# Optimization experiments

Measured on AMD Instinct MI355X. Metric: run time of the kernel, lower is better.

Reference implementation:

```python
import jax, jax.numpy as jnp
import numpy as np
import math

B, TQ, TK = 64, 1024, 512
CONV_CH, EMBED_DIM, ATT_HID = 512, 512, 512
KEY_POS_RATE = 1.385
QUERY_POS_RATE = 1.0
POSITION_WEIGHT = 1.0


def sin_pos_enc(positions, w, d):
    # positions: [B, T] int, padding_idx=0 maps to zero vector.
    # pe[..., 2i]   = sin(w*pos / 10000^(2i/d))
    # pe[..., 2i+1] = cos(w*pos / 10000^(2i/d))
    i = jnp.arange(d)
    inv_freq = jnp.power(jnp.float32(10000.0), -(2.0 * (i // 2).astype(jnp.float32)) / d)  # [d]
    ang = (positions.astype(jnp.float32) * w)[..., None] * inv_freq  # [B, T, d]
    pe = jnp.where(i % 2 == 0, jnp.sin(ang), jnp.cos(ang))
    return jnp.where((positions == 0)[..., None], jnp.float32(0.0), pe)


def setup_inputs() -> dict:
    key = jax.random.key(0)
    ks = jax.random.split(key, 12)
    s = 0.02
    inp = {
        "query": jax.random.normal(ks[0], (B, TQ, CONV_CH), jnp.float32),
        "keys": jax.random.normal(ks[1], (B, TK, EMBED_DIM), jnp.float32),
        "values": jax.random.normal(ks[2], (B, TK, EMBED_DIM), jnp.float32),
        # 1-based positions (0 is the padding index of SinusoidalEncoding)
        "text_positions": jnp.broadcast_to(jnp.arange(1, TK + 1, dtype=jnp.int64), (B, TK)),
        "frame_positions": jnp.broadcast_to(jnp.arange(1, TQ + 1, dtype=jnp.int64), (B, TQ)),
        # pad mask over keys: last 64 text positions are padding
        "mask": jnp.broadcast_to(jnp.arange(TK) >= (TK - 64), (B, TK)),
        "Wq": jax.random.normal(ks[3], (CONV_CH, ATT_HID), jnp.float32) * s,
        "bq": jnp.zeros((ATT_HID,), jnp.float32),
        "Wk": jax.random.normal(ks[4], (EMBED_DIM, ATT_HID), jnp.float32) * s,
        "bk": jnp.zeros((ATT_HID,), jnp.float32),
        "Wv": jax.random.normal(ks[5], (EMBED_DIM, ATT_HID), jnp.float32) * s,
        "bv": jnp.zeros((ATT_HID,), jnp.float32),
        "Wo": jax.random.normal(ks[6], (ATT_HID, CONV_CH), jnp.float32) * s,
        "bo": jnp.zeros((CONV_CH,), jnp.float32),
    }
    return inp


def reference(query, keys, values, text_positions, frame_positions, mask,
              Wq, bq, Wk, bk, Wv, bv, Wo, bo):
    # positional-bias injection (position_weight = 1.0)
    keys = keys + POSITION_WEIGHT * sin_pos_enc(text_positions, KEY_POS_RATE, EMBED_DIM)[:, :keys.shape[1], :]
    query = query + POSITION_WEIGHT * sin_pos_enc(frame_positions, QUERY_POS_RATE, CONV_CH)[:, :frame_positions.shape[-1], :]

    v = values @ Wv + bv            # [B, TK, H]
    k = keys @ Wk + bk              # [B, TK, H]
    q = query @ Wq + bq             # [B, TQ, H]

    scores = jnp.einsum('bqh,bkh->bqk', q, k)               # [B, TQ, TK]
    scores = jnp.where(mask[:, None, :], -jnp.inf, scores)
    attn = jax.nn.softmax(scores, axis=2)
    # dropout is a no-op in eval mode
    x = jnp.einsum('bqk,bkh->bqh', attn, v)
    x = x * jnp.float32(math.sqrt(1.0 / v.shape[1]))
    out = x @ Wo + bo               # [B, TQ, conv_channels]
    return out, attn
```

## Files before the change

### kernel.cpp

```cpp
#include <hip/hip_runtime.h>
#include <stdint.h>

#define DEVI __device__ __forceinline__

typedef __attribute__((ext_vector_type(4))) float     f4v;
typedef __attribute__((ext_vector_type(8))) _Float16  h8;
typedef __attribute__((ext_vector_type(4))) _Float16  h4;
typedef unsigned int  u32;

static constexpr int   TQ = 1024, TKN = 512;
static constexpr float KEY_RATE = 1.385f;
static constexpr float QRY_RATE = 1.0f;
static constexpr float SCALE    = 0.04419417382415922f;
static constexpr float INVC     = 0.05190512648261504f;

static constexpr size_t OFF_MM   = 0;
static constexpr size_t OFF_NT   = OFF_MM  + (size_t)512*512*2;
static constexpr size_t OFF_WOT  = OFF_NT  + (size_t)512*512*2;
static constexpr size_t OFF_PEQ  = OFF_WOT + (size_t)512*512*4;
static constexpr size_t OFF_W    = OFF_PEQ + (size_t)1024*512*4;
static constexpr size_t OFF_C    = OFF_W   + 512*4;
static constexpr size_t OFF_BQBK = OFF_C   + 512*4;
static constexpr size_t OFF_T    = OFF_BQBK + 256;
static constexpr size_t OFF_KP   = OFF_T   + (size_t)64*512*4;
static constexpr size_t OFF_MKT  = OFF_KP  + (size_t)64*512*512*2;
static constexpr size_t OFF_PT   = OFF_MKT + (size_t)64*512*512*2;
static constexpr size_t WS_NEED  = OFF_PT  + (size_t)64*512*512*2;
static constexpr size_t OFF_A16  = WS_NEED;
static constexpr size_t WS_BIG   = OFF_A16 + (size_t)64*1024*512*2;

#define WAITV(N) asm volatile("s_waitcnt vmcnt(" #N ")" ::: "memory")
#define WAITL()  asm volatile("s_waitcnt lgkmcnt(0)" ::: "memory")
#define SCHEDB() __builtin_amdgcn_sched_barrier(0)
#define BARRAW() __builtin_amdgcn_s_barrier()

DEVI f4v mfma16(h8 a, h8 b, f4v c) {
  return __builtin_amdgcn_mfma_f32_16x16x32_f16(a, b, c, 0, 0, 0);
}

DEVI void gld16(void* lds, const void* g) {
  __builtin_amdgcn_global_load_lds(
      (const __attribute__((address_space(1))) unsigned int*)g,
      (__attribute__((address_space(3))) unsigned int*)lds, 16, 0, 0);
}

DEVI void stage_B(char* Bbuf, const _Float16* B, int k0, int tid) {
#pragma unroll
  for (int it = 0; it < 4; ++it) {
    const int c = (it << 9) + tid;
    const int r = c >> 2, s = c & 3;
    const int sg = s ^ ((r >> 1) & 3);
    gld16(Bbuf + ((size_t)c << 4), B + (size_t)r * 512 + k0 + (sg << 3));
  }
}

DEVI void stage_A16(char* Abuf, const _Float16* A, int k0, int tid) {
  const int r = tid >> 2, s = tid & 3;
  const int sg = s ^ ((r >> 1) & 3);
  gld16(Abuf + ((size_t)tid << 4), A + (size_t)r * 512 + k0 + (sg << 3));
}

DEVI void loads_A32(f4v& x0, f4v& x1, const float* A, const float* add, int k0, int tid) {
  const int r = tid >> 2, c8 = (tid & 3) << 3;
  const float* p = A + (size_t)r * 512 + k0 + c8;
  x0 = *(const f4v*)p; x1 = *(const f4v*)(p + 4);
  if (add) {
    const float* q = add + (size_t)r * 512 + k0 + c8;
    x0 += *(const f4v*)q; x1 += *(const f4v*)(q + 4);
  }
}
DEVI void write_A32(char* Abuf, f4v x0, f4v x1, int tid) {
  const int r = tid >> 2;
  const int slot = (tid & 3) ^ ((r >> 1) & 3);
  h8 o;
#pragma unroll
  for (int i = 0; i < 4; ++i) { o[i] = (_Float16)x0[i]; o[4 + i] = (_Float16)x1[i]; }
  *(h8*)(Abuf + (r << 6) + (slot << 4)) = o;
}

DEVI void read_fragsA(const char* Ab, int wr, int lane, h8 (&a)[4]) {
  const int l15 = lane & 15, hi = lane >> 4;
#pragma unroll
  for (int mi = 0; mi < 4; ++mi) {
    const int r = wr * 64 + mi * 16 + l15;
    a[mi] = *(const h8*)(Ab + (r << 6) + ((hi ^ ((r >> 1) & 3)) << 4));
  }
}
DEVI void read_fragsB(const char* Bb, int wc, int lane, h8 (&b)[8]) {
  const int l15 = lane & 15, hi = lane >> 4;
#pragma unroll
  for (int nj = 0; nj < 8; ++nj) {
    const int g = wc * 128 + nj * 16 + l15;
    b[nj] = *(const h8*)(Bb + (g << 6) + ((hi ^ ((g >> 1) & 3)) << 4));
  }
}

#define MFMA_ALL(a, bf, acc)                                   \
  _Pragma("unroll") for (int mi = 0; mi < 4; ++mi)             \
  _Pragma("unroll") for (int nj = 0; nj < 8; ++nj)             \
      acc[mi][nj] = mfma16(a[mi], bf[nj], acc[mi][nj]);

#define REG_PIPELINE(As, Ad, Bs, acc)                                              \
  {                                                                                \
    char* const Abf[2] = {lds, lds + 8192};                                        \
    char* const Bbf[3] = {lds + 16384, lds + 49152, lds + 81920};                  \
    f4v xa0, xa1, xb0, xb1;                                                        \
    loads_A32(xa0, xa1, As, Ad, 0, tid);                                           \
    loads_A32(xb0, xb1, As, Ad, 32, tid);                                          \
    SCHEDB();                                                                      \
    stage_B(Bbf[0], Bs, 0, tid);                                                   \
    stage_B(Bbf[1], Bs, 32, tid);                                                  \
    WAITV(4);                                                                      \
    write_A32(Abf[0], xa0, xa1, tid);                                              \
    WAITL(); SCHEDB(); BARRAW(); SCHEDB();                                         \
    _Pragma("unroll")                                                              \
    for (int k = 0; k < 16; ++k) {                                                 \
      if (k < 14) {                                                                \
        if ((k & 1) == 0) { loads_A32(xa0, xa1, As, Ad, (k + 2) * 32, tid); }      \
        else              { loads_A32(xb0, xb1, As, Ad, (k + 2) * 32, tid); }      \
        SCHEDB();                                                                  \
        stage_B(Bbf[(k + 2) % 3], Bs, (k + 2) * 32, tid);                          \
      }                                                                            \
      h8 a[4], bf[8];                                                              \
      read_fragsA(Abf[k & 1], wr, lane, a);                                        \
      read_fragsB(Bbf[k % 3], wc, lane, bf);                                       \
      MFMA_ALL(a, bf, acc);                                                        \
      if (k < 15) {                                                                \
        if (k < 14) { WAITV(6); } else { WAITV(0); }                               \
        if ((k & 1) == 0) write_A32(Abf[1], xb0, xb1, tid);                        \
        else              write_A32(Abf[0], xa0, xa1, tid);                        \
        WAITL(); SCHEDB(); BARRAW(); SCHEDB();                                     \
      }                                                                            \
    }                                                                              \
  }

#define GLD_PIPELINE(As, Bs, acc)                                                  \
  {                                                                                \
    char* const Abf[3] = {lds, lds + 8192, lds + 16384};                           \
    char* const Bbf[3] = {lds + 24576, lds + 57344, lds + 90112};                  \
    stage_A16(Abf[0], As, 0, tid);  stage_B(Bbf[0], Bs, 0, tid);                   \
    stage_A16(Abf[1], As, 32, tid); stage_B(Bbf[1], Bs, 32, tid);                  \
    WAITV(5); SCHEDB(); BARRAW(); SCHEDB();                                        \
    _Pragma("unroll")                                                              \
    for (int k = 0; k < 16; ++k) {                                                 \
      if (k < 14) {                                                                \
        stage_A16(Abf[(k + 2) % 3], As, (k + 2) * 32, tid);                        \
        stage_B(Bbf[(k + 2) % 3], Bs, (k + 2) * 32, tid);                          \
      }                                                                            \
      h8 a[4], bf[8];                                                              \
      read_fragsA(Abf[k % 3], wr, lane, a);                                        \
      read_fragsB(Bbf[k % 3], wc, lane, bf);                                       \
      MFMA_ALL(a, bf, acc);                                                        \
      if (k < 14) { WAITV(5); } else if (k == 14) { WAITV(0); }                    \
      if (k < 15) { WAITL(); SCHEDB(); BARRAW(); SCHEDB(); }                       \
    }                                                                              \
  }

DEVI void stage_f32_A(char* Abuf, const float* A, int k0, int tid) {
#pragma unroll
  for (int it = 0; it < 2; ++it) {
    const int idx = (it << 9) + tid;
    const int r = idx >> 3, c4 = idx & 7;
    f4v x = *(const f4v*)(A + (size_t)r * 512 + k0 + (c4 << 2));
    h4 o;
#pragma unroll
    for (int i = 0; i < 4; ++i) o[i] = (_Float16)x[i];
    const int slot = (c4 >> 1) ^ ((r >> 1) & 3);
    *(h4*)(Abuf + (r << 6) + (slot << 4) + ((c4 & 1) << 3)) = o;
  }
}
DEVI void stage_f32_B(char* Bbuf, const float* B, int k0, int tid) {
#pragma unroll
  for (int it = 0; it < 8; ++it) {
    const int idx = (it << 9) + tid;
    const int r = idx >> 3, c4 = idx & 7;
    f4v x = *(const f4v*)(B + (size_t)r * 512 + k0 + (c4 << 2));
    h4 o;
#pragma unroll
    for (int i = 0; i < 4; ++i) o[i] = (_Float16)x[i];
    const int slot = (c4 >> 1) ^ ((r >> 1) & 3);
    *(h4*)(Bbuf + (r << 6) + (slot << 4) + ((c4 & 1) << 3)) = o;
  }
}

__global__ __launch_bounds__(256) void k_prepA(
    const float* __restrict__ Wk, const float* __restrict__ bq,
    const float* __restrict__ bk,
    const float* __restrict__ Wo,
    const void* __restrict__ fpos_raw,
    float* __restrict__ wvec, float* __restrict__ bqbk,
    float* __restrict__ PEQ, float* __restrict__ WoT) {
  const int bid = blockIdx.x, tid = threadIdx.x;
  if (bid < 128) {
    const int wid = tid >> 6, lane = tid & 63;
    const int row = bid * 4 + wid;
    const float* p = Wk + (size_t)row * 512 + lane * 8;
    const f4v a = *(const f4v*)p, c = *(const f4v*)(p + 4);
    const f4v b0 = *(const f4v*)(bq + lane * 8), b1 = *(const f4v*)(bq + lane * 8 + 4);
    float d = a[0]*b0[0]+a[1]*b0[1]+a[2]*b0[2]+a[3]*b0[3]
            + c[0]*b1[0]+c[1]*b1[1]+c[2]*b1[2]+c[3]*b1[3];
#pragma unroll
    for (int off = 32; off; off >>= 1) d += __shfl_xor(d, off);
    if (lane == 0) wvec[row] = d;
  } else if (bid == 128) {
    __shared__ float red[256];
    red[tid] = bq[tid] * bk[tid] + bq[tid + 256] * bk[tid + 256];
    __syncthreads();
    if (tid == 0) { float s = 0.f; for (int h = 0; h < 256; ++h) s += red[h]; bqbk[0] = s; }
  } else if (bid < 129 + 2048) {
    const u32* fp = (const u32*)fpos_raw;
    const bool is64 = (fp[1] == 0);
    const int t = (bid - 129) * 256 + tid;
    const int tq = t >> 9, d = t & 511;
    const int pos = (int)(is64 ? fp[2 * tq] : fp[tq]);
    float pe = 0.f;
    if (pos != 0) {
      const float invf = exp2f(-(float)(d >> 1) * INVC);
      const float ang  = ((float)pos * QRY_RATE) * invf;
      pe = (d & 1) ? cosf(ang) : sinf(ang);
    }
    PEQ[t] = pe;
  } else {
    __shared__ float t[32][33];
    const int local = bid - 2177;
    const int bx = local & 15, by = local >> 4;
    const int tx = tid & 31, ty = tid >> 5;
    const int x = bx * 32 + tx;
#pragma unroll
    for (int j = 0; j < 4; ++j)
      t[ty + 8 * j][tx] = Wo[(size_t)(by * 32 + ty + 8 * j) * 512 + x];
    __syncthreads();
    const int x2 = by * 32 + tx;
#pragma unroll
    for (int j = 0; j < 4; ++j)
      WoT[(size_t)(bx * 32 + ty + 8 * j) * 512 + x2] = t[tx][ty + 8 * j];
  }
}

__global__ __launch_bounds__(512) void k_prepB(
    const float* __restrict__ Wq, const float* __restrict__ Wk,
    const float* __restrict__ WoT, const float* __restrict__ Wv,
    const float* __restrict__ keys, const void* __restrict__ tpos_raw,
    const void* __restrict__ mask_raw,
    const float* __restrict__ wvec, const float* __restrict__ bqbk,
    const float* __restrict__ bv, const float* __restrict__ bo,
    _Float16* __restrict__ Mm, _Float16* __restrict__ Nt,
    _Float16* __restrict__ kp, float* __restrict__ tvec,
    float* __restrict__ cvec) {
  __shared__ char lds[40960];
  const int bid = blockIdx.x, tid = threadIdx.x;
  const int lane = tid & 63, wid = tid >> 6;
  if (bid < 8) {
    char *Ab = lds, *Bb = lds + 8192;
    const int wr = wid >> 2, wc = wid & 3;
    const int x = bid & 3, y = bid >> 2;
    const float* A = (y == 0 ? Wq : WoT) + (size_t)x * 128 * 512;
    const float* B = (y == 0 ? Wk : Wv);
    _Float16* out = (y == 0 ? Mm : Nt) + (size_t)x * 128 * 512;
    f4v acc[4][8] = {};
    for (int ks = 0; ks < 16; ++ks) {
      stage_f32_A(Ab, A, ks * 32, tid);
      stage_f32_B(Bb, B, ks * 32, tid);
      __syncthreads();
      h8 a[4], bf[8];
      read_fragsA(Ab, wr, lane, a);
      read_fragsB(Bb, wc, lane, bf);
      MFMA_ALL(a, bf, acc);
      __syncthreads();
    }
    const int l15 = lane & 15, hi = lane >> 4;
#pragma unroll
    for (int mi = 0; mi < 4; ++mi)
#pragma unroll
      for (int nj = 0; nj < 8; ++nj) {
        const int col = wc * 128 + nj * 16 + l15;
#pragma unroll
        for (int j = 0; j < 4; ++j) {
          const int row = wr * 64 + mi * 16 + hi * 4 + j;
          out[(size_t)row * 512 + col] = (_Float16)acc[mi][nj][j];
        }
      }
  } else if (bid < 4104) {
    const u32* tp = (const u32*)tpos_raw;
    const bool is64 = (tp[1] == 0);
    const int row = (bid - 8) * 8 + wid;
    const int pos = (int)(is64 ? tp[2 * row] : tp[row]);
    const int d0  = lane * 8;
    const float* src = keys + (size_t)row * 512 + d0;
    const f4v a = *(const f4v*)src, b = *(const f4v*)(src + 4);
    float x[8] = {a[0], a[1], a[2], a[3], b[0], b[1], b[2], b[3]};
    if (pos != 0) {
      const float pw = (float)pos * KEY_RATE;
#pragma unroll
      for (int u = 0; u < 4; ++u) {
        const float invf = exp2f(-(float)(lane * 4 + u) * INVC);
        const float ang  = pw * invf;
        x[2*u]   += sinf(ang);
        x[2*u+1] += cosf(ang);
      }
    }
    const f4v w0 = *(const f4v*)(wvec + d0), w1 = *(const f4v*)(wvec + d0 + 4);
    float dot = 0.f;
#pragma unroll
    for (int i = 0; i < 4; ++i) dot += x[i] * w0[i] + x[4+i] * w1[i];
#pragma unroll
    for (int off = 32; off; off >>= 1) dot += __shfl_xor(dot, off);
    if (lane == 0) {
      const u32* m32 = (const u32*)mask_raw;
      const bool is32 = (m32[448] != 0);
      const bool mk = is32 ? (m32[row] != 0)
                           : (((const unsigned char*)mask_raw)[row] != 0);
      tvec[row] = mk ? -1e30f : (dot + bqbk[0]);
    }
    h8 o;
#pragma unroll
    for (int i = 0; i < 8; ++i) o[i] = (_Float16)x[i];
    *(h8*)(kp + (size_t)row * 512 + d0) = o;
  } else {
    const int row = (bid - 4104) * 8 + wid;
    const float* p = WoT + (size_t)row * 512 + lane * 8;
    const f4v a = *(const f4v*)p, c = *(const f4v*)(p + 4);
    const f4v b0 = *(const f4v*)(bv + lane * 8), b1 = *(const f4v*)(bv + lane * 8 + 4);
    float d = a[0]*b0[0]+a[1]*b0[1]+a[2]*b0[2]+a[3]*b0[3]
            + c[0]*b1[0]+c[1]*b1[1]+c[2]*b1[2]+c[3]*b1[3];
#pragma unroll
    for (int off = 32; off; off >>= 1) d += __shfl_xor(d, off);
    if (lane == 0) cvec[row] = SCALE * d + bo[row];
  }
}

__global__ __launch_bounds__(512, 1) void k_mkpv(
    const _Float16* __restrict__ kp, const _Float16* __restrict__ Mm,
    const float* __restrict__ values, const _Float16* __restrict__ Nt,
    _Float16* __restrict__ MKt, _Float16* __restrict__ Pt) {
  __shared__ char lds[122880];
  const int bid = blockIdx.x, tid = threadIdx.x;
  const int lane = tid & 63, wid = tid >> 6;
  const int wr = wid >> 2, wc = wid & 3;
  const int l15 = lane & 15, hi = lane >> 4;
  f4v acc[4][8] = {};
  if (bid < 256) {
    const int tt = bid & 3, b = bid >> 2;
    const _Float16* As = kp + ((size_t)b * TKN + tt * 128) * 512;
    GLD_PIPELINE(As, Mm, acc);
    _Float16* Ob = MKt + (size_t)b * TKN * 512 + (size_t)tt * 128 * 512;
#pragma unroll
    for (int mi = 0; mi < 4; ++mi)
#pragma unroll
      for (int nj = 0; nj < 8; ++nj) {
        const int col = wc * 128 + nj * 16 + l15;
#pragma unroll
        for (int j = 0; j < 4; ++j) {
          const int row = wr * 64 + mi * 16 + hi * 4 + j;
          Ob[(size_t)row * 512 + col] = (_Float16)acc[mi][nj][j];
        }
      }
  } else {
    const int rt = (bid - 256) & 3, b = (bid - 256) >> 2;
    const float* As = values + ((size_t)b * TKN + rt * 128) * 512;
    const float* Ad = nullptr;
    REG_PIPELINE(As, Ad, Nt, acc);
    _Float16* Pb = Pt + (size_t)b * 512 * 512;
#pragma unroll
    for (int mi = 0; mi < 4; ++mi)
#pragma unroll
      for (int nj = 0; nj < 8; ++nj) {
        const int col = wc * 128 + nj * 16 + l15;
        const int t0  = rt * 128 + wr * 64 + mi * 16 + hi * 4;
        h4 o;
#pragma unroll
        for (int j = 0; j < 4; ++j) o[j] = (_Float16)acc[mi][nj][j];
        *(h4*)(Pb + (size_t)col * 512 + t0) = o;
      }
  }
}

__global__ __launch_bounds__(512, 1) void k_scores(
    const float* __restrict__ query, const float* __restrict__ PEQ,
    const _Float16* __restrict__ MKt, const float* __restrict__ tve,
    float* __restrict__ attn, _Float16* __restrict__ a16) {
  __shared__ char lds[114688];
  const int tid = threadIdx.x, lane = tid & 63, wid = tid >> 6;
  const int wr = wid >> 2, wc = wid & 3;
  const int bid = blockIdx.x;
  const int xcd = bid & 7, i = bid >> 3;
  const int qt = i & 7, b = xcd * 8 + (i >> 3);
  const float* As = query + ((size_t)b * TQ + qt * 128) * 512;
  const float* Ad = PEQ + (size_t)(qt * 128) * 512;
  const _Float16* Bs = MKt + (size_t)b * TKN * 512;
  const int l15 = lane & 15, hi = lane >> 4;
  float tv[8];
#pragma unroll
  for (int nj = 0; nj < 8; ++nj) tv[nj] = tve[b * TKN + wc * 128 + nj * 16 + l15];
  f4v acc[4][8] = {};
  REG_PIPELINE(As, Ad, Bs, acc);
  float* red  = (float*)lds;
  float* red2 = (float*)(lds + 2048);
#pragma unroll
  for (int mi = 0; mi < 4; ++mi)
#pragma unroll
    for (int nj = 0; nj < 8; ++nj) {
      const float t = tv[nj];
#pragma unroll
      for (int j = 0; j < 4; ++j) acc[mi][nj][j] += t;
    }
  float mrow[4][4];
#pragma unroll
  for (int mi = 0; mi < 4; ++mi)
#pragma unroll
    for (int j = 0; j < 4; ++j) {
      float m = acc[mi][0][j];
#pragma unroll
      for (int nj = 1; nj < 8; ++nj) m = fmaxf(m, acc[mi][nj][j]);
      m = fmaxf(m, __shfl_xor(m, 1)); m = fmaxf(m, __shfl_xor(m, 2));
      m = fmaxf(m, __shfl_xor(m, 4)); m = fmaxf(m, __shfl_xor(m, 8));
      mrow[mi][j] = m;
    }
  __syncthreads();
  if (l15 == 0) {
#pragma unroll
    for (int mi = 0; mi < 4; ++mi)
#pragma unroll
      for (int j = 0; j < 4; ++j)
        red[(wr * 64 + mi * 16 + hi * 4 + j) * 4 + wc] = mrow[mi][j];
  }
  __syncthreads();
#pragma unroll
  for (int mi = 0; mi < 4; ++mi)
#pragma unroll
    for (int j = 0; j < 4; ++j) {
      const f4v rv = *(const f4v*)(red + (wr * 64 + mi * 16 + hi * 4 + j) * 4);
      mrow[mi][j] = fmaxf(fmaxf(rv[0], rv[1]), fmaxf(rv[2], rv[3]));
    }
  float srow[4][4];
#pragma unroll
  for (int mi = 0; mi < 4; ++mi)
#pragma unroll
    for (int j = 0; j < 4; ++j) {
      float s = 0.f;
      const float m = mrow[mi][j];
#pragma unroll
      for (int nj = 0; nj < 8; ++nj) {
        const float e = expf(acc[mi][nj][j] - m);
        acc[mi][nj][j] = e; s += e;
      }
      s += __shfl_xor(s, 1); s += __shfl_xor(s, 2);
      s += __shfl_xor(s, 4); s += __shfl_xor(s, 8);
      srow[mi][j] = s;
    }
  if (l15 == 0) {
#pragma unroll
    for (int mi = 0; mi < 4; ++mi)
#pragma unroll
      for (int j = 0; j < 4; ++j)
        red2[(wr * 64 + mi * 16 + hi * 4 + j) * 4 + wc] = srow[mi][j];
  }
  __syncthreads();
  float* Ao = attn + ((size_t)b * TQ + qt * 128) * 512;
  _Float16* Ah = a16 ? a16 + ((size_t)b * TQ + qt * 128) * 512 : nullptr;
#pragma unroll
  for (int mi = 0; mi < 4; ++mi)
#pragma unroll
    for (int j = 0; j < 4; ++j) {
      const int row = wr * 64 + mi * 16 + hi * 4 + j;
      const f4v sv = *(const f4v*)(red2 + row * 4);
      const float rinv = 1.f / (sv[0] + sv[1] + sv[2] + sv[3]);
#pragma unroll
      for (int nj = 0; nj < 8; ++nj) {
        const float v = acc[mi][nj][j] * rinv;
        const int col = wc * 128 + nj * 16 + l15;
        Ao[(size_t)row * 512 + col] = v;
        if (Ah) Ah[(size_t)row * 512 + col] = (_Float16)v;
      }
    }
}

template <int A16P>
__global__ __launch_bounds__(512, 1) void k_final(
    const float* __restrict__ attn, const _Float16* __restrict__ attn16,
    const _Float16* __restrict__ Pt, const float* __restrict__ cvec,
    float* __restrict__ outp) {
  __shared__ char lds[122880];
  const int tid = threadIdx.x, lane = tid & 63, wid = tid >> 6;
  const int wr = wid >> 2, wc = wid & 3;
  const int bid = blockIdx.x;
  const int xcd = bid & 7, i = bid >> 3;
  const int qt = i & 7, b = xcd * 8 + (i >> 3);
  const _Float16* Bs = Pt + (size_t)b * 512 * 512;
  const int l15 = lane & 15, hi = lane >> 4;
  f4v acc[4][8] = {};
  if (A16P) {
    const _Float16* As = attn16 + ((size_t)b * TQ + qt * 128) * 512;
    GLD_PIPELINE(As, Bs, acc);
  } else {
    const float* As = attn + ((size_t)b * TQ + qt * 128) * 512;
    const float* Ad = nullptr;
    REG_PIPELINE(As, Ad, Bs, acc);
  }
  float cv[8];
#pragma unroll
  for (int nj = 0; nj < 8; ++nj) cv[nj] = cvec[wc * 128 + nj * 16 + l15];
  float* Ob = outp + ((size_t)b * TQ + qt * 128) * 512;
#pragma unroll
  for (int mi = 0; mi < 4; ++mi)
#pragma unroll
    for (int nj = 0; nj < 8; ++nj) {
      const int col = wc * 128 + nj * 16 + l15;
#pragma unroll
      for (int j = 0; j < 4; ++j) {
        const int row = wr * 64 + mi * 16 + hi * 4 + j;
        Ob[(size_t)row * 512 + col] = SCALE * acc[mi][nj][j] + cv[nj];
      }
    }
}

extern "C" void kernel_launch(void* const* d_in, const int* in_sizes, int n_in,
                              void* d_out, int out_size, void* d_ws, size_t ws_size,
                              hipStream_t stream) {
  (void)in_sizes; (void)n_in; (void)out_size;
  if (ws_size < WS_NEED) return;
  const bool big = (ws_size >= WS_BIG);

  const float* query  = (const float*)d_in[0];
  const float* keys   = (const float*)d_in[1];
  const float* values = (const float*)d_in[2];
  const void*  tpos   = d_in[3];
  const void*  fpos   = d_in[4];
  const void*  mask   = d_in[5];
  const float* Wq = (const float*)d_in[6];
  const float* bq = (const float*)d_in[7];
  const float* Wk = (const float*)d_in[8];
  const float* bk = (const float*)d_in[9];
  const float* Wv = (const float*)d_in[10];
  const float* bv = (const float*)d_in[11];
  const float* Wo = (const float*)d_in[12];
  const float* bo = (const float*)d_in[13];

  char* ws = (char*)d_ws;
  _Float16* Mm   = (_Float16*)(ws + OFF_MM);
  _Float16* Nt   = (_Float16*)(ws + OFF_NT);
  float*    WoT  = (float*)   (ws + OFF_WOT);
  float*    PEQ  = (float*)   (ws + OFF_PEQ);
  float*    wvec = (float*)   (ws + OFF_W);
  float*    cvec = (float*)   (ws + OFF_C);
  float*    bqbk = (float*)   (ws + OFF_BQBK);
  float*    tvec = (float*)   (ws + OFF_T);
  _Float16* kp   = (_Float16*)(ws + OFF_KP);
  _Float16* MKt  = (_Float16*)(ws + OFF_MKT);
  _Float16* Pt   = (_Float16*)(ws + OFF_PT);
  _Float16* a16  = big ? (_Float16*)(ws + OFF_A16) : nullptr;

  float* outp = (float*)d_out;
  float* attn = outp + (size_t)64 * TQ * 512;

  k_prepA<<<2433, 256, 0, stream>>>(Wk, bq, bk, Wo, fpos, wvec, bqbk, PEQ, WoT);
  k_prepB<<<4168, 512, 0, stream>>>(Wq, Wk, WoT, Wv, keys, tpos, mask,
                                    wvec, bqbk, bv, bo, Mm, Nt, kp, tvec, cvec);
  k_mkpv <<<512, 512, 0, stream>>>(kp, Mm, values, Nt, MKt, Pt);
  k_scores<<<512, 512, 0, stream>>>(query, PEQ, MKt, tvec, attn, a16);
  if (big) k_final<1><<<512, 512, 0, stream>>>(attn, a16, Pt, cvec, outp);
  else     k_final<0><<<512, 512, 0, stream>>>(attn, a16, Pt, cvec, outp);
}
```

Baseline: 302.5 us.

## Fuse score softmax and output projection into a single kernel

Merges the scores/softmax kernel with the final attention-times-P GEMM. The normalized probabilities are kept in registers as fp16, written into swizzled LDS slices in two halves, and multiplied against streamed Pt tiles within the same block. This removes the fp16 attention round-trip through global memory, the re-read in a separate kernel, and one launch. In exchange it adds extra barriers and a serialized second GEMM phase per block, and register pressure rises because both accumulator sets are live.

New measurement: 407.4 us. +34.7%, slower.

```diff
diff --git a/kernel.cpp b/kernel.cpp
--- a/kernel.cpp
+++ b/kernel.cpp
@@ -19,15 +19,13 @@
 static constexpr size_t OFF_WOT  = OFF_NT  + (size_t)512*512*2;
 static constexpr size_t OFF_PEQ  = OFF_WOT + (size_t)512*512*4;
 static constexpr size_t OFF_W    = OFF_PEQ + (size_t)1024*512*4;
-static constexpr size_t OFF_C    = OFF_W   + 512*4;
-static constexpr size_t OFF_BQBK = OFF_C   + 512*4;
+static constexpr size_t OFF_C    = OFF_W   + 2048;
+static constexpr size_t OFF_BQBK = OFF_C   + 2048;
 static constexpr size_t OFF_T    = OFF_BQBK + 256;
 static constexpr size_t OFF_KP   = OFF_T   + (size_t)64*512*4;
 static constexpr size_t OFF_MKT  = OFF_KP  + (size_t)64*512*512*2;
 static constexpr size_t OFF_PT   = OFF_MKT + (size_t)64*512*512*2;
 static constexpr size_t WS_NEED  = OFF_PT  + (size_t)64*512*512*2;
-static constexpr size_t OFF_A16  = WS_NEED;
-static constexpr size_t WS_BIG   = OFF_A16 + (size_t)64*1024*512*2;
 
 #define WAITV(N) asm volatile("s_waitcnt vmcnt(" #N ")" ::: "memory")
 #define WAITL()  asm volatile("s_waitcnt lgkmcnt(0)" ::: "memory")
@@ -375,10 +373,11 @@
   }
 }
 
-__global__ __launch_bounds__(512, 1) void k_scores(
+__global__ __launch_bounds__(512, 1) void k_out(
     const float* __restrict__ query, const float* __restrict__ PEQ,
     const _Float16* __restrict__ MKt, const float* __restrict__ tve,
-    float* __restrict__ attn, _Float16* __restrict__ a16) {
+    const _Float16* __restrict__ Pt, const float* __restrict__ cvec,
+    float* __restrict__ attn, float* __restrict__ outp) {
   __shared__ char lds[114688];
   const int tid = threadIdx.x, lane = tid & 63, wid = tid >> 6;
   const int wr = wid >> 2, wc = wid & 3;
@@ -388,12 +387,15 @@
   const float* As = query + ((size_t)b * TQ + qt * 128) * 512;
   const float* Ad = PEQ + (size_t)(qt * 128) * 512;
   const _Float16* Bs = MKt + (size_t)b * TKN * 512;
+  const _Float16* PtB = Pt + (size_t)b * 512 * 512;
   const int l15 = lane & 15, hi = lane >> 4;
   float tv[8];
 #pragma unroll
   for (int nj = 0; nj < 8; ++nj) tv[nj] = tve[b * TKN + wc * 128 + nj * 16 + l15];
+
   f4v acc[4][8] = {};
   REG_PIPELINE(As, Ad, Bs, acc);
+
   float* red  = (float*)lds;
   float* red2 = (float*)(lds + 2048);
 #pragma unroll
@@ -456,8 +458,9 @@
         red2[(wr * 64 + mi * 16 + hi * 4 + j) * 4 + wc] = srow[mi][j];
   }
   __syncthreads();
+
   float* Ao = attn + ((size_t)b * TQ + qt * 128) * 512;
-  _Float16* Ah = a16 ? a16 + ((size_t)b * TQ + qt * 128) * 512 : nullptr;
+  h4 pk[4][8];
 #pragma unroll
   for (int mi = 0; mi < 4; ++mi)
 #pragma unroll
@@ -468,34 +471,43 @@
 #pragma unroll
       for (int nj = 0; nj < 8; ++nj) {
         const float v = acc[mi][nj][j] * rinv;
-        const int col = wc * 128 + nj * 16 + l15;
-        Ao[(size_t)row * 512 + col] = v;
-        if (Ah) Ah[(size_t)row * 512 + col] = (_Float16)v;
-      }
-    }
-}
-
-template <int A16P>
-__global__ __launch_bounds__(512, 1) void k_final(
-    const float* __restrict__ attn, const _Float16* __restrict__ attn16,
-    const _Float16* __restrict__ Pt, const float* __restrict__ cvec,
-    float* __restrict__ outp) {
-  __shared__ char lds[122880];
-  const int tid = threadIdx.x, lane = tid & 63, wid = tid >> 6;
-  const int wr = wid >> 2, wc = wid & 3;
-  const int bid = blockIdx.x;
-  const int xcd = bid & 7, i = bid >> 3;
-  const int qt = i & 7, b = xcd * 8 + (i >> 3);
-  const _Float16* Bs = Pt + (size_t)b * 512 * 512;
-  const int l15 = lane & 15, hi = lane >> 4;
-  f4v acc[4][8] = {};
-  if (A16P) {
-    const _Float16* As = attn16 + ((size_t)b * TQ + qt * 128) * 512;
-    GLD_PIPELINE(As, Bs, acc);
-  } else {
-    const float* As = attn + ((size_t)b * TQ + qt * 128) * 512;
-    const float* Ad = nullptr;
-    REG_PIPELINE(As, Ad, Bs, acc);
+        Ao[(size_t)row * 512 + wc * 128 + nj * 16 + l15] = v;
+        pk[mi][nj][j] = (_Float16)v;
+      }
+    }
+
+  f4v oacc[4][8] = {};
+  char* const Ptb1 = lds + 65536;
+#pragma unroll
+  for (int h = 0; h < 2; ++h) {
+    __syncthreads();
+    if ((wc >> 1) == h) {
+#pragma unroll
+      for (int nj = 0; nj < 8; ++nj) {
+        const int sl  = ((wc & 1) << 2) + (nj >> 1);
+        const int c32 = ((nj & 1) << 4) | l15;
+#pragma unroll
+        for (int mi = 0; mi < 4; ++mi)
+#pragma unroll
+          for (int j = 0; j < 4; ++j) {
+            const int r = wr * 64 + mi * 16 + hi * 4 + j;
+            const int addr = sl * 8192 + (r << 6)
+                           + (((c32 >> 3) ^ ((r >> 1) & 3)) << 4) + ((c32 & 7) << 1);
+            *(_Float16*)(lds + addr) = pk[mi][nj][j];
+          }
+      }
+    }
+#pragma unroll
+    for (int sl = 0; sl < 8; ++sl) {
+      const int s = h * 8 + sl;
+      stage_B(Ptb1, PtB, s * 32, tid);
+      __syncthreads();
+      h8 pa[4], pb[8];
+      read_fragsA(lds + sl * 8192, wr, lane, pa);
+      read_fragsB(Ptb1, wc, lane, pb);
+      MFMA_ALL(pa, pb, oacc);
+      __syncthreads();
+    }
   }
   float cv[8];
 #pragma unroll
@@ -509,7 +521,7 @@
 #pragma unroll
       for (int j = 0; j < 4; ++j) {
         const int row = wr * 64 + mi * 16 + hi * 4 + j;
-        Ob[(size_t)row * 512 + col] = SCALE * acc[mi][nj][j] + cv[nj];
+        Ob[(size_t)row * 512 + col] = SCALE * oacc[mi][nj][j] + cv[nj];
       }
     }
 }
@@ -519,7 +531,6 @@
                               hipStream_t stream) {
   (void)in_sizes; (void)n_in; (void)out_size;
   if (ws_size < WS_NEED) return;
-  const bool big = (ws_size >= WS_BIG);
 
   const float* query  = (const float*)d_in[0];
   const float* keys   = (const float*)d_in[1];
@@ -548,7 +559,6 @@
   _Float16* kp   = (_Float16*)(ws + OFF_KP);
   _Float16* MKt  = (_Float16*)(ws + OFF_MKT);
   _Float16* Pt   = (_Float16*)(ws + OFF_PT);
-  _Float16* a16  = big ? (_Float16*)(ws + OFF_A16) : nullptr;
 
   float* outp = (float*)d_out;
   float* attn = outp + (size_t)64 * TQ * 512;
@@ -557,7 +567,5 @@
   k_prepB<<<4168, 512, 0, stream>>>(Wq, Wk, WoT, Wv, keys, tpos, mask,
                                     wvec, bqbk, bv, bo, Mm, Nt, kp, tvec, cvec);
   k_mkpv <<<512, 512, 0, stream>>>(kp, Mm, values, Nt, MKt, Pt);
-  k_scores<<<512, 512, 0, stream>>>(query, PEQ, MKt, tvec, attn, a16);
-  if (big) k_final<1><<<512, 512, 0, stream>>>(attn, a16, Pt, cvec, outp);
-  else     k_final<0><<<512, 512, 0, stream>>>(attn, a16, Pt, cvec, outp);
-}
+  k_out  <<<512, 512, 0, stream>>>(query, PEQ, MKt, tvec, Pt, cvec, attn, outp);
+}
```

## Halve GEMM tiles to 64 rows with 256-thread blocks at two blocks per CU

Applied to the files above, without the earlier changes.

The three MFMA GEMM kernels change from 128-row tiles on 512-thread blocks to 64-row tiles on 256-thread blocks, launched as 1024 blocks with two resident per CU. LDS drops to 72KB per block. The hand-tuned three-stage pipeline with explicit vmcnt waits and raw barriers becomes a plain double buffer synchronised with __syncthreads. The aim is to hide latency through cross-block occupancy rather than deep in-block prefetching. In exchange, every B tile is loaded twice as often per output row, and each block gets less overlap of its own.

Measured after the change: 343.1 us. 13.4% more time.

```diff
diff --git a/kernel.cpp b/kernel.cpp
--- a/kernel.cpp
+++ b/kernel.cpp
@@ -19,8 +19,8 @@
 static constexpr size_t OFF_WOT  = OFF_NT  + (size_t)512*512*2;
 static constexpr size_t OFF_PEQ  = OFF_WOT + (size_t)512*512*4;
 static constexpr size_t OFF_W    = OFF_PEQ + (size_t)1024*512*4;
-static constexpr size_t OFF_C    = OFF_W   + 512*4;
-static constexpr size_t OFF_BQBK = OFF_C   + 512*4;
+static constexpr size_t OFF_C    = OFF_W   + 2048;
+static constexpr size_t OFF_BQBK = OFF_C   + 2048;
 static constexpr size_t OFF_T    = OFF_BQBK + 256;
 static constexpr size_t OFF_KP   = OFF_T   + (size_t)64*512*4;
 static constexpr size_t OFF_MKT  = OFF_KP  + (size_t)64*512*512*2;
@@ -29,11 +29,6 @@
 static constexpr size_t OFF_A16  = WS_NEED;
 static constexpr size_t WS_BIG   = OFF_A16 + (size_t)64*1024*512*2;
 
-#define WAITV(N) asm volatile("s_waitcnt vmcnt(" #N ")" ::: "memory")
-#define WAITL()  asm volatile("s_waitcnt lgkmcnt(0)" ::: "memory")
-#define SCHEDB() __builtin_amdgcn_sched_barrier(0)
-#define BARRAW() __builtin_amdgcn_s_barrier()
-
 DEVI f4v mfma16(h8 a, h8 b, f4v c) {
   return __builtin_amdgcn_mfma_f32_16x16x32_f16(a, b, c, 0, 0, 0);
 }
@@ -46,8 +41,8 @@
 
 DEVI void stage_B(char* Bbuf, const _Float16* B, int k0, int tid) {
 #pragma unroll
-  for (int it = 0; it < 4; ++it) {
-    const int c = (it << 9) + tid;
+  for (int it = 0; it < 8; ++it) {
+    const int c = (it << 8) + tid;
     const int r = c >> 2, s = c & 3;
     const int sg = s ^ ((r >> 1) & 3);
     gld16(Bbuf + ((size_t)c << 4), B + (size_t)r * 512 + k0 + (sg << 3));
@@ -102,57 +97,48 @@
 
 #define REG_PIPELINE(As, Ad, Bs, acc)                                              \
   {                                                                                \
-    char* const Abf[2] = {lds, lds + 8192};                                        \
-    char* const Bbf[3] = {lds + 16384, lds + 49152, lds + 81920};                  \
-    f4v xa0, xa1, xb0, xb1;                                                        \
-    loads_A32(xa0, xa1, As, Ad, 0, tid);                                           \
-    loads_A32(xb0, xb1, As, Ad, 32, tid);                                          \
-    SCHEDB();                                                                      \
+    char* const Abf[2] = {lds, lds + 4096};                                        \
+    char* const Bbf[2] = {lds + 8192, lds + 40960};                                \
+    f4v x0, x1;                                                                    \
+    loads_A32(x0, x1, As, Ad, 0, tid);                                             \
     stage_B(Bbf[0], Bs, 0, tid);                                                   \
-    stage_B(Bbf[1], Bs, 32, tid);                                                  \
-    WAITV(4);                                                                      \
-    write_A32(Abf[0], xa0, xa1, tid);                                              \
-    WAITL(); SCHEDB(); BARRAW(); SCHEDB();                                         \
+    write_A32(Abf[0], x0, x1, tid);                                                \
+    __syncthreads();                                                               \
     _Pragma("unroll")                                                              \
     for (int k = 0; k < 16; ++k) {                                                 \
-      if (k < 14) {                                                                \
-        if ((k & 1) == 0) { loads_A32(xa0, xa1, As, Ad, (k + 2) * 32, tid); }      \
-        else              { loads_A32(xb0, xb1, As, Ad, (k + 2) * 32, tid); }      \
-        SCHEDB();                                                                  \
-        stage_B(Bbf[(k + 2) % 3], Bs, (k + 2) * 32, tid);                          \
+      if (k < 15) {                                                                \
+        loads_A32(x0, x1, As, Ad, (k + 1) * 32, tid);                              \
+        stage_B(Bbf[(k + 1) & 1], Bs, (k + 1) * 32, tid);                          \
       }                                                                            \
       h8 a[4], bf[8];                                                              \
-      read_fragsA(Abf[k & 1], wr, lane, a);                                        \
-      read_fragsB(Bbf[k % 3], wc, lane, bf);                                       \
+      read_fragsA(Abf[k & 1], 0, lane, a);                                         \
+      read_fragsB(Bbf[k & 1], wc, lane, bf);                                       \
       MFMA_ALL(a, bf, acc);                                                        \
       if (k < 15) {                                                                \
-        if (k < 14) { WAITV(6); } else { WAITV(0); }                               \
-        if ((k & 1) == 0) write_A32(Abf[1], xb0, xb1, tid);                        \
-        else              write_A32(Abf[0], xa0, xa1, tid);                        \
-        WAITL(); SCHEDB(); BARRAW(); SCHEDB();                                     \
+        write_A32(Abf[(k + 1) & 1], x0, x1, tid);                                  \
+        __syncthreads();                                                           \
       }                                                                            \
     }                                                                              \
   }
 
 #define GLD_PIPELINE(As, Bs, acc)                                                  \
   {                                                                                \
-    char* const Abf[3] = {lds, lds + 8192, lds + 16384};                           \
-    char* const Bbf[3] = {lds + 24576, lds + 57344, lds + 90112};                  \
-    stage_A16(Abf[0], As, 0, tid);  stage_B(Bbf[0], Bs, 0, tid);                   \
-    stage_A16(Abf[1], As, 32, tid); stage_B(Bbf[1], Bs, 32, tid);                  \
-    WAITV(5); SCHEDB(); BARRAW(); SCHEDB();                                        \
+    char* const Abf[2] = {lds, lds + 4096};                                        \
+    char* const Bbf[2] = {lds + 8192, lds + 40960};                                \
+    stage_A16(Abf[0], As, 0, tid);                                                 \
+    stage_B(Bbf[0], Bs, 0, tid);                                                   \
+    __syncthreads();                                                               \
     _Pragma("unroll")                                                              \
     for (int k = 0; k < 16; ++k) {                                                 \
-      if (k < 14) {                                                                \
-        stage_A16(Abf[(k + 2) % 3], As, (k + 2) * 32, tid);                        \
-        stage_B(Bbf[(k + 2) % 3], Bs, (k + 2) * 32, tid);                          \
+      if (k < 15) {                                                                \
+        stage_A16(Abf[(k + 1) & 1], As, (k + 1) * 32, tid);                        \
+        stage_B(Bbf[(k + 1) & 1], Bs, (k + 1) * 32, tid);                          \
       }                                                                            \
       h8 a[4], bf[8];                                                              \
-      read_fragsA(Abf[k % 3], wr, lane, a);                                        \
-      read_fragsB(Bbf[k % 3], wc, lane, bf);                                       \
+      read_fragsA(Abf[k & 1], 0, lane, a);                                         \
+      read_fragsB(Bbf[k & 1], wc, lane, bf);                                       \
       MFMA_ALL(a, bf, acc);                                                        \
-      if (k < 14) { WAITV(5); } else if (k == 14) { WAITV(0); }                    \
-      if (k < 15) { WAITL(); SCHEDB(); BARRAW(); SCHEDB(); }                       \
+      if (k < 15) __syncthreads();                                                 \
     }                                                                              \
   }
 
@@ -329,21 +315,20 @@
   }
 }
 
-__global__ __launch_bounds__(512, 1) void k_mkpv(
+__global__ __launch_bounds__(256, 2) void k_mkpv(
     const _Float16* __restrict__ kp, const _Float16* __restrict__ Mm,
     const float* __restrict__ values, const _Float16* __restrict__ Nt,
     _Float16* __restrict__ MKt, _Float16* __restrict__ Pt) {
-  __shared__ char lds[122880];
+  __shared__ char lds[73728];
   const int bid = blockIdx.x, tid = threadIdx.x;
-  const int lane = tid & 63, wid = tid >> 6;
-  const int wr = wid >> 2, wc = wid & 3;
+  const int lane = tid & 63, wc = (tid >> 6) & 3;
   const int l15 = lane & 15, hi = lane >> 4;
   f4v acc[4][8] = {};
-  if (bid < 256) {
-    const int tt = bid & 3, b = bid >> 2;
-    const _Float16* As = kp + ((size_t)b * TKN + tt * 128) * 512;
+  if (bid < 512) {
+    const int tt = bid & 7, b = bid >> 3;
+    const _Float16* As = kp + ((size_t)b * TKN + tt * 64) * 512;
     GLD_PIPELINE(As, Mm, acc);
-    _Float16* Ob = MKt + (size_t)b * TKN * 512 + (size_t)tt * 128 * 512;
+    _Float16* Ob = MKt + (size_t)b * TKN * 512 + (size_t)tt * 64 * 512;
 #pragma unroll
     for (int mi = 0; mi < 4; ++mi)
 #pragma unroll
@@ -351,13 +336,14 @@
         const int col = wc * 128 + nj * 16 + l15;
 #pragma unroll
         for (int j = 0; j < 4; ++j) {
-          const int row = wr * 64 + mi * 16 + hi * 4 + j;
+          const int row = mi * 16 + hi * 4 + j;
           Ob[(size_t)row * 512 + col] = (_Float16)acc[mi][nj][j];
         }
       }
   } else {
-    const int rt = (bid - 256) & 3, b = (bid - 256) >> 2;
-    const float* As = values + ((size_t)b * TKN + rt * 128) * 512;
+    const int idx = bid - 512;
+    const int rt = idx & 7, b = idx >> 3;
+    const float* As = values + ((size_t)b * TKN + rt * 64) * 512;
     const float* Ad = nullptr;
     REG_PIPELINE(As, Ad, Nt, acc);
     _Float16* Pb = Pt + (size_t)b * 512 * 512;
@@ -366,7 +352,7 @@
 #pragma unroll
       for (int nj = 0; nj < 8; ++nj) {
         const int col = wc * 128 + nj * 16 + l15;
-        const int t0  = rt * 128 + wr * 64 + mi * 16 + hi * 4;
+        const int t0  = rt * 64 + mi * 16 + hi * 4;
         h4 o;
 #pragma unroll
         for (int j = 0; j < 4; ++j) o[j] = (_Float16)acc[mi][nj][j];
@@ -375,18 +361,17 @@
   }
 }
 
-__global__ __launch_bounds__(512, 1) void k_scores(
+__global__ __launch_bounds__(256, 2) void k_scores(
     const float* __restrict__ query, const float* __restrict__ PEQ,
     const _Float16* __restrict__ MKt, const float* __restrict__ tve,
     float* __restrict__ attn, _Float16* __restrict__ a16) {
-  __shared__ char lds[114688];
-  const int tid = threadIdx.x, lane = tid & 63, wid = tid >> 6;
-  const int wr = wid >> 2, wc = wid & 3;
+  __shared__ char lds[73728];
+  const int tid = threadIdx.x, lane = tid & 63, wc = (tid >> 6) & 3;
   const int bid = blockIdx.x;
   const int xcd = bid & 7, i = bid >> 3;
-  const int qt = i & 7, b = xcd * 8 + (i >> 3);
-  const float* As = query + ((size_t)b * TQ + qt * 128) * 512;
-  const float* Ad = PEQ + (size_t)(qt * 128) * 512;
+  const int qt = i & 15, b = xcd * 8 + (i >> 4);
+  const float* As = query + ((size_t)b * TQ + qt * 64) * 512;
+  const float* Ad = PEQ + (size_t)(qt * 64) * 512;
   const _Float16* Bs = MKt + (size_t)b * TKN * 512;
   const int l15 = lane & 15, hi = lane >> 4;
   float tv[8];
@@ -395,7 +380,7 @@
   f4v acc[4][8] = {};
   REG_PIPELINE(As, Ad, Bs, acc);
   float* red  = (float*)lds;
-  float* red2 = (float*)(lds + 2048);
+  float* red2 = (float*)(lds + 1024);
 #pragma unroll
   for (int mi = 0; mi < 4; ++mi)
 #pragma unroll
@@ -422,14 +407,14 @@
     for (int mi = 0; mi < 4; ++mi)
 #pragma unroll
       for (int j = 0; j < 4; ++j)
-        red[(wr * 64 + mi * 16 + hi * 4 + j) * 4 + wc] = mrow[mi][j];
+        red[(mi * 16 + hi * 4 + j) * 4 + wc] = mrow[mi][j];
   }
   __syncthreads();
 #pragma unroll
   for (int mi = 0; mi < 4; ++mi)
 #pragma unroll
     for (int j = 0; j < 4; ++j) {
-      const f4v rv = *(const f4v*)(red + (wr * 64 + mi * 16 + hi * 4 + j) * 4);
+      const f4v rv = *(const f4v*)(red + (mi * 16 + hi * 4 + j) * 4);
       mrow[mi][j] = fmaxf(fmaxf(rv[0], rv[1]), fmaxf(rv[2], rv[3]));
     }
   float srow[4][4];
@@ -453,16 +438,16 @@
     for (int mi = 0; mi < 4; ++mi)
 #pragma unroll
       for (int j = 0; j < 4; ++j)
-        red2[(wr * 64 + mi * 16 + hi * 4 + j) * 4 + wc] = srow[mi][j];
+        red2[(mi * 16 + hi * 4 + j) * 4 + wc] = srow[mi][j];
   }
   __syncthreads();
-  float* Ao = attn + ((size_t)b * TQ + qt * 128) * 512;
-  _Float16* Ah = a16 ? a16 + ((size_t)b * TQ + qt * 128) * 512 : nullptr;
+  float* Ao = attn + ((size_t)b * TQ + qt * 64) * 512;
+  _Float16* Ah = a16 ? a16 + ((size_t)b * TQ + qt * 64) * 512 : nullptr;
 #pragma unroll
   for (int mi = 0; mi < 4; ++mi)
 #pragma unroll
     for (int j = 0; j < 4; ++j) {
-      const int row = wr * 64 + mi * 16 + hi * 4 + j;
+      const int row = mi * 16 + hi * 4 + j;
       const f4v sv = *(const f4v*)(red2 + row * 4);
       const float rinv = 1.f / (sv[0] + sv[1] + sv[2] + sv[3]);
 #pragma unroll
@@ -476,31 +461,30 @@
 }
 
 template <int A16P>
-__global__ __launch_bounds__(512, 1) void k_final(
+__global__ __launch_bounds__(256, 2) void k_final(
     const float* __restrict__ attn, const _Float16* __restrict__ attn16,
     const _Float16* __restrict__ Pt, const float* __restrict__ cvec,
     float* __restrict__ outp) {
-  __shared__ char lds[122880];
-  const int tid = threadIdx.x, lane = tid & 63, wid = tid >> 6;
-  const int wr = wid >> 2, wc = wid & 3;
+  __shared__ char lds[73728];
+  const int tid = threadIdx.x, lane = tid & 63, wc = (tid >> 6) & 3;
   const int bid = blockIdx.x;
   const int xcd = bid & 7, i = bid >> 3;
-  const int qt = i & 7, b = xcd * 8 + (i >> 3);
+  const int qt = i & 15, b = xcd * 8 + (i >> 4);
   const _Float16* Bs = Pt + (size_t)b * 512 * 512;
   const int l15 = lane & 15, hi = lane >> 4;
   f4v acc[4][8] = {};
   if (A16P) {
-    const _Float16* As = attn16 + ((size_t)b * TQ + qt * 128) * 512;
+    const _Float16* As = attn16 + ((size_t)b * TQ + qt * 64) * 512;
     GLD_PIPELINE(As, Bs, acc);
   } else {
-    const float* As = attn + ((size_t)b * TQ + qt * 128) * 512;
+    const float* As = attn + ((size_t)b * TQ + qt * 64) * 512;
     const float* Ad = nullptr;
     REG_PIPELINE(As, Ad, Bs, acc);
   }
   float cv[8];
 #pragma unroll
   for (int nj = 0; nj < 8; ++nj) cv[nj] = cvec[wc * 128 + nj * 16 + l15];
-  float* Ob = outp + ((size_t)b * TQ + qt * 128) * 512;
+  float* Ob = outp + ((size_t)b * TQ + qt * 64) * 512;
 #pragma unroll
   for (int mi = 0; mi < 4; ++mi)
 #pragma unroll
@@ -508,7 +492,7 @@
       const int col = wc * 128 + nj * 16 + l15;
 #pragma unroll
       for (int j = 0; j < 4; ++j) {
-        const int row = wr * 64 + mi * 16 + hi * 4 + j;
+        const int row = mi * 16 + hi * 4 + j;
         Ob[(size_t)row * 512 + col] = SCALE * acc[mi][nj][j] + cv[nj];
       }
     }
@@ -556,8 +540,8 @@
   k_prepA<<<2433, 256, 0, stream>>>(Wk, bq, bk, Wo, fpos, wvec, bqbk, PEQ, WoT);
   k_prepB<<<4168, 512, 0, stream>>>(Wq, Wk, WoT, Wv, keys, tpos, mask,
                                     wvec, bqbk, bv, bo, Mm, Nt, kp, tvec, cvec);
-  k_mkpv <<<512, 512, 0, stream>>>(kp, Mm, values, Nt, MKt, Pt);
-  k_scores<<<512, 512, 0, stream>>>(query, PEQ, MKt, tvec, attn, a16);
-  if (big) k_final<1><<<512, 512, 0, stream>>>(attn, a16, Pt, cvec, outp);
-  else     k_final<0><<<512, 512, 0, stream>>>(attn, a16, Pt, cvec, outp);
-}
+  k_mkpv <<<1024, 256, 0, stream>>>(kp, Mm, values, Nt, MKt, Pt);
+  k_scores<<<1024, 256, 0, stream>>>(query, PEQ, MKt, tvec, attn, a16);
+  if (big) k_final<1><<<1024, 256, 0, stream>>>(attn, a16, Pt, cvec, outp);
+  else     k_final<0><<<1024, 256, 0, stream>>>(attn, a16, Pt, cvec, outp);
+}
```
